# Kernel optimization log

Hardware: AMD Instinct MI355X
Metric: run time of the kernel (lower is better)

## Reference

```python
import jax, jax.numpy as jnp
import numpy as np

N, E, IN_CH, C, H, L, NCLS = 4096, 131072, 512, 256, 4, 3, 2
DH = C // H  # MHA head dim


def _ln(x, g, b, eps=1e-5):
    mu = x.mean(-1, keepdims=True)
    var = ((x - mu) ** 2).mean(-1, keepdims=True)
    return (x - mu) * jax.lax.rsqrt(var + eps) * g + b


def _gelu(x):
    return jax.nn.gelu(x, approximate=False)  # torch nn.GELU default (erf)


def _gatv2(x, src, dst, wl, wr, att, b):
    # x: [N,C]; wl/wr: [H*C, C]; att: [H,C]; b: [C]
    xl = (x @ wl.T).reshape(N, H, C)  # source transform
    e = jax.nn.leaky_relu(xl[src] + (x @ wr.T).reshape(N, H, C)[dst], 0.2)  # [Et,H,C]
    score = jnp.einsum('ehc,hc->eh', e, att)  # [Et,H]
    m = jax.ops.segment_max(score, dst, num_segments=N)
    ex = jnp.exp(score - m[dst])
    denom = jax.ops.segment_sum(ex, dst, num_segments=N)
    alpha = ex / denom[dst]  # segment softmax over incoming edges
    out = jax.ops.segment_sum(alpha[:, :, None] * xl[src], dst, num_segments=N)
    return out.mean(axis=1) + b  # concat=False -> head mean


def _mha(x, in_w, in_b, out_w, out_b):
    qkv = x @ in_w.T + in_b  # [N,3C]
    q, k, v = [t.reshape(N, H, DH) for t in jnp.split(qkv, 3, axis=-1)]
    scores = jnp.einsum('nhd,mhd->hnm', q, k) / np.sqrt(DH)
    probs = jax.nn.softmax(scores, axis=-1)
    o = jnp.einsum('hnm,mhd->nhd', probs, v).reshape(N, C)
    return o @ out_w.T + out_b


def setup_inputs() -> dict:
    key = jax.random.key(0)
    ks = iter(jax.random.split(key, 64))
    s = lambda shape, sc=0.05: jax.random.normal(next(ks), shape, jnp.float32) * sc
    d = {
        'x': jax.random.normal(next(ks), (N, IN_CH), jnp.float32),
        'edge_index': jax.random.randint(next(ks), (2, E), 0, N, jnp.int32),
        'in_w': s((C, IN_CH)), 'in_b': jnp.zeros((C,), jnp.float32),
        'gat_wl': s((L, H * C, C)), 'gat_wr': s((L, H * C, C)),
        'gat_att': s((L, H, C)), 'gat_b': jnp.zeros((L, C), jnp.float32),
        'mha_in_w': s((L, 3 * C, C)), 'mha_in_b': jnp.zeros((L, 3 * C), jnp.float32),
        'mha_out_w': s((L, C, C)), 'mha_out_b': jnp.zeros((L, C), jnp.float32),
        'ln1_g': jnp.ones((L, C), jnp.float32), 'ln1_b': jnp.zeros((L, C), jnp.float32),
        'ln2_g': jnp.ones((L, C), jnp.float32), 'ln2_b': jnp.zeros((L, C), jnp.float32),
        'ln3_g': jnp.ones((L, C), jnp.float32), 'ln3_b': jnp.zeros((L, C), jnp.float32),
        'ffn_w1': s((L, 2 * C, C)), 'ffn_b1': jnp.zeros((L, 2 * C), jnp.float32),
        'ffn_w2': s((L, C, 2 * C)), 'ffn_b2': jnp.zeros((L, C), jnp.float32),
        'out_w1': s((C, C)), 'out_b1': jnp.zeros((C,), jnp.float32),
        'out_w2': s((NCLS, C)), 'out_b2': jnp.zeros((NCLS,), jnp.float32),
    }
    return d


def reference(x, edge_index, in_w, in_b, gat_wl, gat_wr, gat_att, gat_b,
              mha_in_w, mha_in_b, mha_out_w, mha_out_b,
              ln1_g, ln1_b, ln2_g, ln2_b, ln3_g, ln3_b,
              ffn_w1, ffn_b1, ffn_w2, ffn_b2,
              out_w1, out_b1, out_w2, out_b2):
    # add self loops (PyG GATv2Conv default)
    loop = jnp.arange(N, dtype=edge_index.dtype)
    src = jnp.concatenate([edge_index[0], loop])
    dst = jnp.concatenate([edge_index[1], loop])

    h = x @ in_w.T + in_b  # input_proj
    for l in range(L):
        local = _gatv2(h, src, dst, gat_wl[l], gat_wr[l], gat_att[l], gat_b[l])
        h = _ln(h + local, ln1_g[l], ln1_b[l])
        attn = _mha(h, mha_in_w[l], mha_in_b[l], mha_out_w[l], mha_out_b[l])
        h = _ln(h + attn, ln2_g[l], ln2_b[l])
        ffn = _gelu(h @ ffn_w1[l].T + ffn_b1[l]) @ ffn_w2[l].T + ffn_b2[l]
        h = _ln(h + ffn, ln3_g[l], ln3_b[l])
    h = _gelu(h @ out_w1.T + out_b1)
    return h @ out_w2.T + out_b2
```

## Files before the change

### kernel.cpp

```cpp
#include <hip/hip_runtime.h>
#include <cstdint>
#include <cstddef>

typedef unsigned short u16;
typedef __bf16 bf16x8 __attribute__((ext_vector_type(8)));
typedef float f32x4 __attribute__((ext_vector_type(4)));

constexpr int kN  = 4096;
constexpr int kE  = 131072;
constexpr int kET = kE + kN;
constexpr int kIn = 512;
constexpr int kC  = 256;
constexpr int kL  = 3;

constexpr int NSPLIT = 4;
constexpr int KSPAN  = kN / NSPLIT;
constexpr int NSTEP  = KSPAN / 64;

__device__ __forceinline__ u16 f2bf(float f) {
    unsigned u = __builtin_bit_cast(unsigned, f);
    u += 0x7fffu + ((u >> 16) & 1u);
    return (u16)(u >> 16);
}
__device__ __forceinline__ float bf2f(u16 s) {
    unsigned u = ((unsigned)s) << 16;
    return __builtin_bit_cast(float, u);
}
__device__ __forceinline__ float gelu_erf(float x) {
    return 0.5f * x * (1.f + erff(x * 0.70710678118654752f));
}
__device__ __forceinline__ void gload_lds16(const u16* gsrc, u16* ldst) {
    __builtin_amdgcn_global_load_lds(
        (const __attribute__((address_space(1))) unsigned int*)gsrc,
        (__attribute__((address_space(3))) unsigned int*)ldst, 16, 0, 0);
}
__device__ __forceinline__ float dpp_ror_add16(float x) {
    int t;
    t = __builtin_amdgcn_update_dpp(0, __builtin_bit_cast(int, x), 0x121, 0xf, 0xf, true);
    x += __builtin_bit_cast(float, t);
    t = __builtin_amdgcn_update_dpp(0, __builtin_bit_cast(int, x), 0x122, 0xf, 0xf, true);
    x += __builtin_bit_cast(float, t);
    t = __builtin_amdgcn_update_dpp(0, __builtin_bit_cast(int, x), 0x124, 0xf, 0xf, true);
    x += __builtin_bit_cast(float, t);
    t = __builtin_amdgcn_update_dpp(0, __builtin_bit_cast(int, x), 0x128, 0xf, 0xf, true);
    x += __builtin_bit_cast(float, t);
    return x;
}
__device__ __forceinline__ void unpack8(uint4 u, float* x) {
    x[0] = __builtin_bit_cast(float, u.x << 16);
    x[1] = __builtin_bit_cast(float, u.x & 0xffff0000u);
    x[2] = __builtin_bit_cast(float, u.y << 16);
    x[3] = __builtin_bit_cast(float, u.y & 0xffff0000u);
    x[4] = __builtin_bit_cast(float, u.z << 16);
    x[5] = __builtin_bit_cast(float, u.z & 0xffff0000u);
    x[6] = __builtin_bit_cast(float, u.w << 16);
    x[7] = __builtin_bit_cast(float, u.w & 0xffff0000u);
}

__global__ void cast_f2b(const float* __restrict__ src, u16* __restrict__ dst, int n4) {
    int i = blockIdx.x * blockDim.x + threadIdx.x;
    if (i >= n4) return;
    float4 v = ((const float4*)src)[i];
    ushort4 o;
    o.x = f2bf(v.x); o.y = f2bf(v.y); o.z = f2bf(v.z); o.w = f2bf(v.w);
    ((ushort4*)dst)[i] = o;
}

__global__ void csr_count(const int* __restrict__ ei, int* __restrict__ cnt) {
    int e = blockIdx.x * 256 + threadIdx.x;
    if (e >= kET) return;
    int d = (e < kE) ? ei[kE + e] : (e - kE);
    atomicAdd(cnt + d, 1);
}

__global__ __launch_bounds__(1024) void csr_scan(int* __restrict__ cnt_cur, int* __restrict__ off) {
    __shared__ int lds[1024];
    int t = threadIdx.x;
    int c[4], s = 0;
#pragma unroll
    for (int j = 0; j < 4; ++j) { c[j] = cnt_cur[t * 4 + j]; s += c[j]; }
    lds[t] = s;
    __syncthreads();
    for (int d = 1; d < 1024; d <<= 1) {
        int v = (t >= d) ? lds[t - d] : 0;
        __syncthreads();
        lds[t] += v;
        __syncthreads();
    }
    int excl = lds[t] - s;
#pragma unroll
    for (int j = 0; j < 4; ++j) { off[t * 4 + j] = excl; cnt_cur[t * 4 + j] = excl; excl += c[j]; }
    if (t == 1023) off[4096] = excl;
}

__global__ void csr_scatter(const int* __restrict__ ei, int* __restrict__ cur, int* __restrict__ csrc) {
    int e = blockIdx.x * 256 + threadIdx.x;
    if (e >= kET) return;
    int s, d;
    if (e < kE) { s = ei[e]; d = ei[kE + e]; } else { s = d = e - kE; }
    int pos = atomicAdd(cur + d, 1);
    csrc[pos] = s;
}

template <int BM, int K, int ACT, int WF32, int WBF16>
__global__ __launch_bounds__(256) void gemm_st(
    const u16* __restrict__ A, const u16* __restrict__ W,
    const float* __restrict__ bias, float* __restrict__ Cf,
    u16* __restrict__ Cb, int N) {
    constexpr int BK = 32;
    constexpr int NK = K / BK;
    constexpr int MF = BM / 32;
    int tid = threadIdx.x;
    int w = tid >> 6, lane = tid & 63;
    int wr = w >> 1, wc = w & 1;
    int g = lane >> 4, r = lane & 15;
    int bm = blockIdx.y * BM;
    int bn = blockIdx.x * 64;
    __shared__ __align__(16) u16 Ab[2][BM * BK];
    __shared__ __align__(16) u16 Bb[2][64 * BK];
    int srow = w * 16 + (lane >> 2);
    int scol = (lane & 3) * 8;
    auto stage = [&](int buf, int k0) {
#pragma unroll
        for (int i = 0; i < BM / 64; ++i)
            gload_lds16(A + (size_t)(bm + i * 64 + srow) * K + k0 + scol,
                        &Ab[buf][(i * 64 + w * 16) * BK]);
        gload_lds16(W + (size_t)(bn + srow) * K + k0 + scol, &Bb[buf][w * 16 * BK]);
    };
    f32x4 acc[MF][2] = {};
    stage(0, 0);
    __syncthreads();
    for (int st = 0; st < NK; ++st) {
        int cur = st & 1;
        if (st + 1 < NK) stage(cur ^ 1, (st + 1) * BK);
        const u16* Al = &Ab[cur][0];
        const u16* Bl = &Bb[cur][0];
        bf16x8 bf[2];
#pragma unroll
        for (int u = 0; u < 2; ++u)
            bf[u] = *(const bf16x8*)(Bl + (wc * 32 + u * 16 + r) * BK + g * 8);
#pragma unroll
        for (int t = 0; t < MF; ++t) {
            bf16x8 af = *(const bf16x8*)(Al + (wr * (BM / 2) + t * 16 + r) * BK + g * 8);
#pragma unroll
            for (int u = 0; u < 2; ++u)
                acc[t][u] = __builtin_amdgcn_mfma_f32_16x16x32_bf16(af, bf[u], acc[t][u], 0, 0, 0);
        }
        __syncthreads();
    }
    int r0 = bm + wr * (BM / 2) + g * 4;
    int c0 = bn + wc * 32 + r;
#pragma unroll
    for (int t = 0; t < MF; ++t)
#pragma unroll
        for (int u = 0; u < 2; ++u)
#pragma unroll
            for (int e = 0; e < 4; ++e) {
                int row = r0 + t * 16 + e, col = c0 + u * 16;
                float v = acc[t][u][e];
                if (bias) v += bias[col];
                if (ACT == 1) v = gelu_erf(v);
                if (WF32) Cf[(size_t)row * N + col] = v;
                if (WBF16) Cb[(size_t)row * N + col] = f2bf(v);
            }
}

__global__ __launch_bounds__(256) void ln_res(
    const float* hin, const float* add,
    const float* __restrict__ g, const float* __restrict__ b,
    float* hout, u16* __restrict__ hbf) {
    int row = blockIdx.x * 4 + (threadIdx.x >> 6);
    int lane = threadIdx.x & 63;
    const float4 x4 = *(const float4*)(hin + (size_t)row * kC + lane * 4);
    const float4 a4 = *(const float4*)(add + (size_t)row * kC + lane * 4);
    float v[4] = {x4.x + a4.x, x4.y + a4.y, x4.z + a4.z, x4.w + a4.w};
    float s = v[0] + v[1] + v[2] + v[3];
    for (int d = 1; d < 64; d <<= 1) s += __shfl_xor(s, d);
    float mu = s * (1.f / kC);
    float q = 0.f;
#pragma unroll
    for (int j = 0; j < 4; ++j) { float d = v[j] - mu; q += d * d; }
    for (int d = 1; d < 64; d <<= 1) q += __shfl_xor(q, d);
    float rstd = rsqrtf(q * (1.f / kC) + 1e-5f);
    const float4 g4 = *(const float4*)(g + lane * 4);
    const float4 b4 = *(const float4*)(b + lane * 4);
    float y0 = (v[0] - mu) * rstd * g4.x + b4.x;
    float y1 = (v[1] - mu) * rstd * g4.y + b4.y;
    float y2 = (v[2] - mu) * rstd * g4.z + b4.z;
    float y3 = (v[3] - mu) * rstd * g4.w + b4.w;
    *(float4*)(hout + (size_t)row * kC + lane * 4) = make_float4(y0, y1, y2, y3);
    ushort4 o; o.x = f2bf(y0); o.y = f2bf(y1); o.z = f2bf(y2); o.w = f2bf(y3);
    *(ushort4*)(hbf + (size_t)row * kC + lane * 4) = o;
}

__global__ __launch_bounds__(256) void gat_agg(
    const u16* __restrict__ xg,
    const float* __restrict__ att, const float* __restrict__ gb,
    const int* __restrict__ off, const int* __restrict__ srcs,
    float* __restrict__ outloc) {
    int n = blockIdx.x;
    int w = threadIdx.x >> 6, lane = threadIdx.x & 63;
    int q = lane >> 4, t = lane & 15;
    int cb = w * 256 + t * 16;

    uint4 xru0 = *(const uint4*)(xg + (size_t)n * 2048 + 1024 + cb);
    uint4 xru1 = *(const uint4*)(xg + (size_t)n * 2048 + 1024 + cb + 8);
    float xrv[16];
    unpack8(xru0, xrv); unpack8(xru1, xrv + 8);
    float att6[16], att4[16];
#pragma unroll
    for (int j = 0; j < 16; j += 4) {
        float4 a4 = *(const float4*)(att + cb + j);
        att6[j] = 0.6f * a4.x; att6[j + 1] = 0.6f * a4.y;
        att6[j + 2] = 0.6f * a4.z; att6[j + 3] = 0.6f * a4.w;
        att4[j] = (2.f / 3.f) * att6[j]; att4[j + 1] = (2.f / 3.f) * att6[j + 1];
        att4[j + 2] = (2.f / 3.f) * att6[j + 2]; att4[j + 3] = (2.f / 3.f) * att6[j + 3];
    }

    int i0 = off[n], i1 = off[n + 1];
    float m = -1e30f, ls = 0.f;
    float acc[16] = {};
    int i = i0 + q;
    uint4 p0, p1;
    if (i < i1) {
        int s = srcs[i];
        p0 = *(const uint4*)(xg + (size_t)s * 2048 + cb);
        p1 = *(const uint4*)(xg + (size_t)s * 2048 + cb + 8);
    }
    while (i < i1) {
        uint4 c0 = p0, c1 = p1;
        int inext = i + 4;
        if (inext < i1) {
            int s2 = srcs[inext];
            p0 = *(const uint4*)(xg + (size_t)s2 * 2048 + cb);
            p1 = *(const uint4*)(xg + (size_t)s2 * 2048 + cb + 8);
        }
        float x[16];
        unpack8(c0, x); unpack8(c1, x + 8);
        float p = 0.f;
#pragma unroll
        for (int j = 0; j < 16; ++j) {
            float e = x[j] + xrv[j];
            p = fmaf(att6[j], e, p);
            p = fmaf(att4[j], __builtin_fabsf(e), p);
        }
        p = dpp_ror_add16(p);
        if (p > m) {
            float c = __expf(m - p);
            ls = ls * c + 1.f;
#pragma unroll
            for (int j = 0; j < 16; ++j) acc[j] = acc[j] * c + x[j];
            m = p;
        } else {
            float pw = __expf(p - m);
            ls += pw;
#pragma unroll
            for (int j = 0; j < 16; ++j) acc[j] = fmaf(pw, x[j], acc[j]);
        }
        i = inext;
    }
    float mm = fmaxf(m, __shfl_xor(m, 16));
    mm = fmaxf(mm, __shfl_xor(mm, 32));
    float c = __expf(m - mm);
    ls *= c;
    ls += __shfl_xor(ls, 16);
    ls += __shfl_xor(ls, 32);
#pragma unroll
    for (int j = 0; j < 16; ++j) {
        float a = acc[j] * c;
        a += __shfl_xor(a, 16);
        a += __shfl_xor(a, 32);
        acc[j] = a;
    }
    float inv = 1.f / ls;
    __shared__ float red[4][256];
    if (q == 0) {
#pragma unroll
        for (int j = 0; j < 16; ++j) red[w][t * 16 + j] = acc[j] * inv;
    }
    __syncthreads();
    int cc = threadIdx.x;
    float vsum = 0.25f * (red[0][cc] + red[1][cc] + red[2][cc] + red[3][cc]) + gb[cc];
    outloc[(size_t)n * kC + cc] = vsum;
}

__global__ __launch_bounds__(256) void qkv_repack(
    const u16* __restrict__ qkvb, u16* __restrict__ Qb, u16* __restrict__ Kb,
    u16* __restrict__ VTb) {
    int h = blockIdx.y;
    int n0 = blockIdx.x * 64;
    int t = threadIdx.x;
    int nr = t >> 2, cb = (t & 3) * 16;
    const u16* src = qkvb + (size_t)(n0 + nr) * 768 + h * 64 + cb;
    u16* qd = Qb + ((size_t)h * kN + n0 + nr) * 64 + cb;
    u16* kd = Kb + ((size_t)h * kN + n0 + nr) * 64 + cb;
    __shared__ u16 lds[64][72];
    constexpr float QS = 0.125f * 1.4426950408889634f;
#pragma unroll
    for (int j = 0; j < 16; j += 4) {
        ushort4 q4 = *(const ushort4*)(src + j);
        ushort4 k4 = *(const ushort4*)(src + 256 + j);
        ushort4 v4 = *(const ushort4*)(src + 512 + j);
        ushort4 qo;
        qo.x = f2bf(bf2f(q4.x) * QS); qo.y = f2bf(bf2f(q4.y) * QS);
        qo.z = f2bf(bf2f(q4.z) * QS); qo.w = f2bf(bf2f(q4.w) * QS);
        *(ushort4*)(qd + j) = qo;
        *(ushort4*)(kd + j) = k4;
        *(ushort4*)(&lds[nr][cb + j]) = v4;
    }
    __syncthreads();
    int d = t >> 2, nb = (t & 3) * 16;
    u16* vd = VTb + ((size_t)h * 64 + d) * kN + n0 + nb;
#pragma unroll
    for (int j = 0; j < 16; j += 4) {
        ushort4 vo;
        vo.x = lds[nb + j + 0][d];
        vo.y = lds[nb + j + 1][d];
        vo.z = lds[nb + j + 2][d];
        vo.w = lds[nb + j + 3][d];
        *(ushort4*)(vd + j) = vo;
    }
}

__global__ __launch_bounds__(256, 4) void mha_mfma2(
    const u16* __restrict__ Qb, const u16* __restrict__ Kb,
    const u16* __restrict__ VTb, float* __restrict__ opart, float* __restrict__ mlpart) {
    int qt = blockIdx.x, head = blockIdx.y, sp = blockIdx.z;
    int tid = threadIdx.x;
    int w = tid >> 6, lane = tid & 63;
    int g = lane >> 4, r = lane & 15;
    int q0 = qt * 64;
    const u16* Qh = Qb + ((size_t)head * kN + q0 + w * 16) * 64;
    const u16* Kh = Kb + (size_t)head * kN * 64;
    const u16* VTh = VTb + (size_t)head * 64 * kN;
    __shared__ u16 Kt[2][64 * 64];
    __shared__ u16 Vt[2][64 * 64];
    __shared__ u16 plds[4][16 * 64];
    int srow = w * 8 + (lane >> 3);
    int schunk = ((lane & 7) ^ ((lane >> 3) & 7)) * 8;
    int kbase = sp * KSPAN;

    bf16x8 qf0 = *(const bf16x8*)(Qh + r * 64 + g * 8);
    bf16x8 qf1 = *(const bf16x8*)(Qh + r * 64 + 32 + g * 8);

    auto stage = [&](int buf, int k0) {
#pragma unroll
        for (int i = 0; i < 2; ++i) {
            int row = i * 32 + srow;
            gload_lds16(Kh + (size_t)(k0 + row) * 64 + schunk, &Kt[buf][(i * 32 + w * 8) * 64]);
            gload_lds16(VTh + (size_t)row * kN + k0 + schunk, &Vt[buf][(i * 32 + w * 8) * 64]);
        }
    };

    f32x4 o[4] = {};
    float m = -3.0e38f, l = 0.f;

    stage(0, kbase);
    __syncthreads();

    int rx = r & 7;
    for (int st = 0; st < NSTEP; ++st) {
        int cur = st & 1;
        if (st + 1 < NSTEP) stage(cur ^ 1, kbase + (st + 1) * 64);
        const u16* Kl = &Kt[cur][0];
        const u16* Vl = &Vt[cur][0];
        f32x4 stt[4] = {};
#pragma unroll
        for (int t = 0; t < 4; ++t) {
            bf16x8 kf0 = *(const bf16x8*)(Kl + (16 * t + r) * 64 + ((0 + g) ^ rx) * 8);
            bf16x8 kf1 = *(const bf16x8*)(Kl + (16 * t + r) * 64 + ((4 + g) ^ rx) * 8);
            stt[t] = __builtin_amdgcn_mfma_f32_16x16x32_bf16(kf0, qf0, stt[t], 0, 0, 0);
            stt[t] = __builtin_amdgcn_mfma_f32_16x16x32_bf16(kf1, qf1, stt[t], 0, 0, 0);
        }
        float pm = stt[0][0];
#pragma unroll
        for (int t = 0; t < 4; ++t)
#pragma unroll
            for (int e = 0; e < 4; ++e) pm = fmaxf(pm, stt[t][e]);
        pm = fmaxf(pm, __shfl_xor(pm, 16));
        pm = fmaxf(pm, __shfl_xor(pm, 32));
        float mn = fmaxf(m, pm);
        float corr = __builtin_amdgcn_exp2f(m - mn);
        float ls = 0.f;
        float p[4][4];
#pragma unroll
        for (int t = 0; t < 4; ++t)
#pragma unroll
            for (int e = 0; e < 4; ++e) { p[t][e] = __builtin_amdgcn_exp2f(stt[t][e] - mn); ls += p[t][e]; }
        ls += __shfl_xor(ls, 16);
        ls += __shfl_xor(ls, 32);
        l = l * corr + ls;
        m = mn;
        float corrq[4];
#pragma unroll
        for (int e = 0; e < 4; ++e) corrq[e] = __shfl(corr, g * 4 + e);
#pragma unroll
        for (int dt = 0; dt < 4; ++dt)
#pragma unroll
            for (int e = 0; e < 4; ++e) o[dt][e] *= corrq[e];
#pragma unroll
        for (int t = 0; t < 4; ++t) {
            ushort4 pk;
            pk.x = f2bf(p[t][0]); pk.y = f2bf(p[t][1]);
            pk.z = f2bf(p[t][2]); pk.w = f2bf(p[t][3]);
            int lc = (2 * t + (g >> 1)) ^ rx;
            *(ushort4*)(&plds[w][r * 64 + lc * 8 + (g & 1) * 4]) = pk;
        }
        bf16x8 pa0 = *(const bf16x8*)(&plds[w][r * 64 + (g ^ rx) * 8]);
        bf16x8 pa1 = *(const bf16x8*)(&plds[w][r * 64 + ((4 + g) ^ rx) * 8]);
#pragma unroll
        for (int dt = 0; dt < 4; ++dt) {
            bf16x8 vf0 = *(const bf16x8*)(Vl + (dt * 16 + r) * 64 + ((0 + g) ^ rx) * 8);
            bf16x8 vf1 = *(const bf16x8*)(Vl + (dt * 16 + r) * 64 + ((4 + g) ^ rx) * 8);
            o[dt] = __builtin_amdgcn_mfma_f32_16x16x32_bf16(pa0, vf0, o[dt], 0, 0, 0);
            o[dt] = __builtin_amdgcn_mfma_f32_16x16x32_bf16(pa1, vf1, o[dt], 0, 0, 0);
        }
        __syncthreads();
    }

    size_t slot = (size_t)(head * 64 + qt) * NSPLIT + sp;
    float* ob = opart + slot * 4096;
#pragma unroll
    for (int dt = 0; dt < 4; ++dt)
#pragma unroll
        for (int e = 0; e < 4; ++e)
            ob[(w * 16 + g * 4 + e) * 64 + dt * 16 + r] = o[dt][e];
    float* mlb = mlpart + slot * 128;
    if (g == 0) { mlb[w * 16 + r] = m; mlb[64 + w * 16 + r] = l; }
}

__global__ __launch_bounds__(256) void mha_merge(
    const float* __restrict__ opart, const float* __restrict__ mlpart,
    u16* __restrict__ attnb) {
    int head = blockIdx.y;
    int q = blockIdx.x * 4 + (threadIdx.x >> 6);
    int d = threadIdx.x & 63;
    int qt = q >> 6, ql = q & 63;
    size_t sb = (size_t)(head * 64 + qt) * NSPLIT;
    float ms[NSPLIT], lsv[NSPLIT];
    float mstar = -3.0e38f;
#pragma unroll
    for (int s = 0; s < NSPLIT; ++s) {
        ms[s] = mlpart[(sb + s) * 128 + ql];
        lsv[s] = mlpart[(sb + s) * 128 + 64 + ql];
        mstar = fmaxf(mstar, ms[s]);
    }
    float acc = 0.f, lsum = 0.f;
#pragma unroll
    for (int s = 0; s < NSPLIT; ++s) {
        float wgt = __builtin_amdgcn_exp2f(ms[s] - mstar);
        lsum += lsv[s] * wgt;
        acc += opart[(sb + s) * 4096 + ql * 64 + d] * wgt;
    }
    attnb[(size_t)q * kC + head * 64 + d] = f2bf(acc / lsum);
}

__global__ __launch_bounds__(256) void final_out(
    const u16* __restrict__ tbf, const float* __restrict__ w2,
    const float* __restrict__ b2, float* __restrict__ out) {
    int row = blockIdx.x * 4 + (threadIdx.x >> 6);
    int lane = threadIdx.x & 63;
    const ushort4 tv = *(const ushort4*)(tbf + (size_t)row * 256 + lane * 4);
    float t0 = bf2f(tv.x), t1 = bf2f(tv.y), t2 = bf2f(tv.z), t3 = bf2f(tv.w);
    const float4 w0 = *(const float4*)(w2 + lane * 4);
    const float4 w1 = *(const float4*)(w2 + 256 + lane * 4);
    float d0 = t0 * w0.x + t1 * w0.y + t2 * w0.z + t3 * w0.w;
    float d1 = t0 * w1.x + t1 * w1.y + t2 * w1.z + t3 * w1.w;
    for (int d = 1; d < 64; d <<= 1) { d0 += __shfl_xor(d0, d); d1 += __shfl_xor(d1, d); }
    if (lane == 0) {
        out[(size_t)row * 2 + 0] = d0 + b2[0];
        out[(size_t)row * 2 + 1] = d1 + b2[1];
    }
}

extern "C" void kernel_launch(void* const* d_in, const int* in_sizes, int n_in,
                              void* d_out, int out_size, void* d_ws, size_t ws_size,
                              hipStream_t stream) {
    (void)in_sizes; (void)n_in; (void)out_size;
    const float* x        = (const float*)d_in[0];
    const int*   ei       = (const int*)d_in[1];
    const float* in_w     = (const float*)d_in[2];
    const float* in_b     = (const float*)d_in[3];
    const float* gat_wl   = (const float*)d_in[4];
    const float* gat_wr   = (const float*)d_in[5];
    const float* gat_att  = (const float*)d_in[6];
    const float* gat_b    = (const float*)d_in[7];
    const float* mha_in_w = (const float*)d_in[8];
    const float* mha_in_b = (const float*)d_in[9];
    const float* mha_out_w= (const float*)d_in[10];
    const float* mha_out_b= (const float*)d_in[11];
    const float* ln1_g = (const float*)d_in[12];
    const float* ln1_b = (const float*)d_in[13];
    const float* ln2_g = (const float*)d_in[14];
    const float* ln2_b = (const float*)d_in[15];
    const float* ln3_g = (const float*)d_in[16];
    const float* ln3_b = (const float*)d_in[17];
    const float* ffn_w1 = (const float*)d_in[18];
    const float* ffn_b1 = (const float*)d_in[19];
    const float* ffn_w2 = (const float*)d_in[20];
    const float* ffn_b2 = (const float*)d_in[21];
    const float* out_w1 = (const float*)d_in[22];
    const float* out_b1 = (const float*)d_in[23];
    const float* out_w2 = (const float*)d_in[24];
    const float* out_b2 = (const float*)d_in[25];
    float* out = (float*)d_out;

    char* ws = (char*)d_ws;
    size_t off = 0;
    auto alloc = [&](size_t bytes) -> void* {
        void* p = (void*)(ws + off);
        off += (bytes + 255) & ~(size_t)255;
        return p;
    };
    float* h     = (float*)alloc((size_t)kN * kC * 4);
    u16*   hbf   = (u16*)  alloc((size_t)kN * kC * 2);
    float* xlb   = (float*)alloc((size_t)kN * 1024 * 4);
    float* xrb   = (float*)alloc((size_t)kN * 1024 * 4);
    float* qkv   = (float*)alloc((size_t)kN * 768 * 4);
    float* locb  = (float*)alloc((size_t)kN * kC * 4);
    u16*   attnb = (u16*)  alloc((size_t)kN * kC * 2);
    u16*   midb  = (u16*)  alloc((size_t)kN * 512 * 2);
    u16*   tbf   = (u16*)  alloc((size_t)kN * kC * 2);
    u16*   xbf   = (u16*)  alloc((size_t)kN * kIn * 2);
    u16*   wbf   = (u16*)  alloc((size_t)3342336 * 2);
    int*   coff  = (int*)  alloc((size_t)4097 * 4);
    int*   ccur  = (int*)  alloc((size_t)4096 * 4);
    int*   csrc  = (int*)  alloc((size_t)kET * 4);
    if (ws_size < off) return;

    u16* xgbf = (u16*)xlb;
    u16* Qb  = (u16*)xlb;
    u16* Kb  = Qb + (size_t)4 * kN * 64;
    u16* VTb = Kb + (size_t)4 * kN * 64;
    u16* qkvb = (u16*)qkv;
    float* opart  = xrb;
    float* mlpart = locb;

    const size_t OFF_INW  = 0;
    const size_t OFF_GAT  = 131072;
    const size_t OFF_MIN  = 1703936;
    const size_t OFF_MOUT = 2293760;
    const size_t OFF_F1   = 2490368;
    const size_t OFF_F2   = 2883584;
    const size_t OFF_O1   = 3276800;

    auto cast = [&](const float* s, u16* d, int n) {
        int n4 = n >> 2;
        cast_f2b<<<dim3((n4 + 255) / 256), dim3(256), 0, stream>>>(s, d, n4);
    };
    cast(x, xbf, kN * kIn);
    cast(in_w, wbf + OFF_INW, kC * kIn);
    for (int l = 0; l < kL; ++l) {
        cast(gat_wl + (size_t)l * 262144, wbf + OFF_GAT + (size_t)l * 524288, 262144);
        cast(gat_wr + (size_t)l * 262144, wbf + OFF_GAT + (size_t)l * 524288 + 262144, 262144);
    }
    cast(mha_in_w, wbf + OFF_MIN, kL * 768 * kC);
    cast(mha_out_w, wbf + OFF_MOUT, kL * kC * kC);
    cast(ffn_w1, wbf + OFF_F1, kL * 512 * kC);
    cast(ffn_w2, wbf + OFF_F2, kL * kC * 512);
    cast(out_w1, wbf + OFF_O1, kC * kC);

    hipMemsetAsync(ccur, 0, 4096 * 4, stream);
    csr_count<<<dim3((kET + 255) / 256), dim3(256), 0, stream>>>(ei, ccur);
    csr_scan<<<dim3(1), dim3(1024), 0, stream>>>(ccur, coff);
    csr_scatter<<<dim3((kET + 255) / 256), dim3(256), 0, stream>>>(ei, ccur, csrc);

    gemm_st<64, 512, 0, 1, 1><<<dim3(kC / 64, kN / 64), dim3(256), 0, stream>>>(
        xbf, wbf + OFF_INW, in_b, h, hbf, kC);

    for (int l = 0; l < kL; ++l) {
        gemm_st<128, 256, 0, 0, 1><<<dim3(2048 / 64, kN / 128), dim3(256), 0, stream>>>(
            hbf, wbf + OFF_GAT + (size_t)l * 524288, nullptr, nullptr, xgbf, 2048);
        gat_agg<<<dim3(kN), dim3(256), 0, stream>>>(
            xgbf, gat_att + (size_t)l * 1024, gat_b + (size_t)l * kC, coff, csrc, locb);
        ln_res<<<dim3(kN / 4), dim3(256), 0, stream>>>(
            h, locb, ln1_g + (size_t)l * kC, ln1_b + (size_t)l * kC, h, hbf);

        gemm_st<128, 256, 0, 0, 1><<<dim3(768 / 64, kN / 128), dim3(256), 0, stream>>>(
            hbf, wbf + OFF_MIN + (size_t)l * 768 * kC, mha_in_b + (size_t)l * 768, nullptr, qkvb, 768);
        qkv_repack<<<dim3(kN / 64, 4), dim3(256), 0, stream>>>(qkvb, Qb, Kb, VTb);
        mha_mfma2<<<dim3(kN / 64, 4, NSPLIT), dim3(256), 0, stream>>>(Qb, Kb, VTb, opart, mlpart);
        mha_merge<<<dim3(kN / 4, 4), dim3(256), 0, stream>>>(opart, mlpart, attnb);
        gemm_st<64, 256, 0, 1, 0><<<dim3(kC / 64, kN / 64), dim3(256), 0, stream>>>(
            attnb, wbf + OFF_MOUT + (size_t)l * kC * kC, mha_out_b + (size_t)l * kC, locb, nullptr, kC);
        ln_res<<<dim3(kN / 4), dim3(256), 0, stream>>>(
            h, locb, ln2_g + (size_t)l * kC, ln2_b + (size_t)l * kC, h, hbf);

        gemm_st<64, 256, 1, 0, 1><<<dim3(512 / 64, kN / 64), dim3(256), 0, stream>>>(
            hbf, wbf + OFF_F1 + (size_t)l * 512 * kC, ffn_b1 + (size_t)l * 512, nullptr, midb, 512);
        gemm_st<64, 512, 0, 1, 0><<<dim3(kC / 64, kN / 64), dim3(256), 0, stream>>>(
            midb, wbf + OFF_F2 + (size_t)l * kC * 512, ffn_b2 + (size_t)l * kC, locb, nullptr, kC);
        ln_res<<<dim3(kN / 4), dim3(256), 0, stream>>>(
            h, locb, ln3_g + (size_t)l * kC, ln3_b + (size_t)l * kC, h, hbf);
    }

    gemm_st<64, 256, 1, 0, 1><<<dim3(kC / 64, kN / 64), dim3(256), 0, stream>>>(
        hbf, wbf + OFF_O1, out_b1, nullptr, tbf, kC);
    final_out<<<dim3(kN / 4), dim3(256), 0, stream>>>(tbf, out_w2, out_b2, out);
}
```

Baseline: 534.4 us.

## Fuse LayerNorm into GAT aggregation, deepen gather prefetch, skip redundant softmax rescale

The GAT aggregation kernel now applies the residual add and LayerNorm itself and writes h and its bf16 copy directly, so one ln_res launch and the locb round trip per layer go away. The edge gather loop prefetches two edges ahead instead of one to hide more gather latency, at the cost of extra registers. In the MHA flash loop, the running-max correction and rescale of the output accumulators run only when some lane's max actually increases. The fused LayerNorm computes variance as E[x^2]-mu^2, which is slightly less numerically robust than the two-pass form it replaces.

Measured after the change: 529.0 us. No clear change (-1.0%).

```diff
diff --git a/kernel.cpp b/kernel.cpp
--- a/kernel.cpp
+++ b/kernel.cpp
@@ -197,7 +197,8 @@
     const u16* __restrict__ xg,
     const float* __restrict__ att, const float* __restrict__ gb,
     const int* __restrict__ off, const int* __restrict__ srcs,
-    float* __restrict__ outloc) {
+    const float* __restrict__ lng, const float* __restrict__ lnb,
+    float* __restrict__ h, u16* __restrict__ hbf) {
     int n = blockIdx.x;
     int w = threadIdx.x >> 6, lane = threadIdx.x & 63;
     int q = lane >> 4, t = lane & 15;
@@ -221,19 +222,24 @@
     float m = -1e30f, ls = 0.f;
     float acc[16] = {};
     int i = i0 + q;
-    uint4 p0, p1;
+    uint4 p0a, p1a, p0b, p1b;
     if (i < i1) {
         int s = srcs[i];
-        p0 = *(const uint4*)(xg + (size_t)s * 2048 + cb);
-        p1 = *(const uint4*)(xg + (size_t)s * 2048 + cb + 8);
+        p0a = *(const uint4*)(xg + (size_t)s * 2048 + cb);
+        p1a = *(const uint4*)(xg + (size_t)s * 2048 + cb + 8);
+    }
+    if (i + 4 < i1) {
+        int s = srcs[i + 4];
+        p0b = *(const uint4*)(xg + (size_t)s * 2048 + cb);
+        p1b = *(const uint4*)(xg + (size_t)s * 2048 + cb + 8);
     }
     while (i < i1) {
-        uint4 c0 = p0, c1 = p1;
-        int inext = i + 4;
-        if (inext < i1) {
-            int s2 = srcs[inext];
-            p0 = *(const uint4*)(xg + (size_t)s2 * 2048 + cb);
-            p1 = *(const uint4*)(xg + (size_t)s2 * 2048 + cb + 8);
+        uint4 c0 = p0a, c1 = p1a;
+        p0a = p0b; p1a = p1b;
+        if (i + 8 < i1) {
+            int s2 = srcs[i + 8];
+            p0b = *(const uint4*)(xg + (size_t)s2 * 2048 + cb);
+            p1b = *(const uint4*)(xg + (size_t)s2 * 2048 + cb + 8);
         }
         float x[16];
         unpack8(c0, x); unpack8(c1, x + 8);
@@ -257,7 +263,7 @@
 #pragma unroll
             for (int j = 0; j < 16; ++j) acc[j] = fmaf(pw, x[j], acc[j]);
         }
-        i = inext;
+        i += 4;
     }
     float mm = fmaxf(m, __shfl_xor(m, 16));
     mm = fmaxf(mm, __shfl_xor(mm, 32));
@@ -274,6 +280,7 @@
     }
     float inv = 1.f / ls;
     __shared__ float red[4][256];
+    __shared__ float rs[8];
     if (q == 0) {
 #pragma unroll
         for (int j = 0; j < 16; ++j) red[w][t * 16 + j] = acc[j] * inv;
@@ -281,7 +288,18 @@
     __syncthreads();
     int cc = threadIdx.x;
     float vsum = 0.25f * (red[0][cc] + red[1][cc] + red[2][cc] + red[3][cc]) + gb[cc];
-    outloc[(size_t)n * kC + cc] = vsum;
+    float v = h[(size_t)n * kC + cc] + vsum;
+    float s1 = v, s2 = v * v;
+    for (int d = 1; d < 64; d <<= 1) { s1 += __shfl_xor(s1, d); s2 += __shfl_xor(s2, d); }
+    if (lane == 0) { rs[w] = s1; rs[4 + w] = s2; }
+    __syncthreads();
+    s1 = rs[0] + rs[1] + rs[2] + rs[3];
+    s2 = rs[4] + rs[5] + rs[6] + rs[7];
+    float mu = s1 * (1.f / kC);
+    float rstd = rsqrtf(s2 * (1.f / kC) - mu * mu + 1e-5f);
+    float y = (v - mu) * rstd * lng[cc] + lnb[cc];
+    h[(size_t)n * kC + cc] = y;
+    hbf[(size_t)n * kC + cc] = f2bf(y);
 }
 
 __global__ __launch_bounds__(256) void qkv_repack(
@@ -379,25 +397,28 @@
             for (int e = 0; e < 4; ++e) pm = fmaxf(pm, stt[t][e]);
         pm = fmaxf(pm, __shfl_xor(pm, 16));
         pm = fmaxf(pm, __shfl_xor(pm, 32));
-        float mn = fmaxf(m, pm);
-        float corr = __builtin_amdgcn_exp2f(m - mn);
+        if (__any(pm > m)) {
+            float mn = fmaxf(m, pm);
+            float corr = __builtin_amdgcn_exp2f(m - mn);
+            l *= corr;
+            float corrq[4];
+#pragma unroll
+            for (int e = 0; e < 4; ++e) corrq[e] = __shfl(corr, g * 4 + e);
+#pragma unroll
+            for (int dt = 0; dt < 4; ++dt)
+#pragma unroll
+                for (int e = 0; e < 4; ++e) o[dt][e] *= corrq[e];
+            m = mn;
+        }
         float ls = 0.f;
         float p[4][4];
 #pragma unroll
         for (int t = 0; t < 4; ++t)
 #pragma unroll
-            for (int e = 0; e < 4; ++e) { p[t][e] = __builtin_amdgcn_exp2f(stt[t][e] - mn); ls += p[t][e]; }
+            for (int e = 0; e < 4; ++e) { p[t][e] = __builtin_amdgcn_exp2f(stt[t][e] - m); ls += p[t][e]; }
         ls += __shfl_xor(ls, 16);
         ls += __shfl_xor(ls, 32);
-        l = l * corr + ls;
-        m = mn;
-        float corrq[4];
-#pragma unroll
-        for (int e = 0; e < 4; ++e) corrq[e] = __shfl(corr, g * 4 + e);
-#pragma unroll
-        for (int dt = 0; dt < 4; ++dt)
-#pragma unroll
-            for (int e = 0; e < 4; ++e) o[dt][e] *= corrq[e];
+        l += ls;
 #pragma unroll
         for (int t = 0; t < 4; ++t) {
             ushort4 pk;
@@ -572,9 +593,8 @@
         gemm_st<128, 256, 0, 0, 1><<<dim3(2048 / 64, kN / 128), dim3(256), 0, stream>>>(
             hbf, wbf + OFF_GAT + (size_t)l * 524288, nullptr, nullptr, xgbf, 2048);
         gat_agg<<<dim3(kN), dim3(256), 0, stream>>>(
-            xgbf, gat_att + (size_t)l * 1024, gat_b + (size_t)l * kC, coff, csrc, locb);
-        ln_res<<<dim3(kN / 4), dim3(256), 0, stream>>>(
-            h, locb, ln1_g + (size_t)l * kC, ln1_b + (size_t)l * kC, h, hbf);
+            xgbf, gat_att + (size_t)l * 1024, gat_b + (size_t)l * kC, coff, csrc,
+            ln1_g + (size_t)l * kC, ln1_b + (size_t)l * kC, h, hbf);
 
         gemm_st<128, 256, 0, 0, 1><<<dim3(768 / 64, kN / 128), dim3(256), 0, stream>>>(
             hbf, wbf + OFF_MIN + (size_t)l * 768 * kC, mha_in_b + (size_t)l * 768, nullptr, qkvb, 768);
```
